# Optimization experiments

Measured on AMD Instinct MI355X. Metric: run time of the kernel, lower is better.

Reference implementation:

```python
import jax, jax.numpy as jnp
import numpy as np

N_ATOMS = 131072
NUM_GS = 128
HIDDEN = 512
N_MOL = 1024


def setup_inputs() -> dict:
    key = jax.random.key(0)
    ks = jax.random.split(key, 16)
    Gs = jax.random.normal(ks[0], (N_ATOMS, NUM_GS), dtype=jnp.float32)
    types = jax.random.randint(ks[1], (N_ATOMS,), 0, 2, dtype=jnp.int32)
    mol_id = jnp.sort(jax.random.randint(ks[2], (N_ATOMS,), 0, N_MOL, dtype=jnp.int32))

    def dense(k, fi, fo):
        return (jax.random.normal(k, (fi, fo), dtype=jnp.float32) / np.float32(np.sqrt(fi)))

    params = {}
    for i, t in enumerate(("A", "B")):
        base = 3 + i * 3
        params[f"W1_{t}"] = dense(ks[base], NUM_GS, HIDDEN)
        params[f"b1_{t}"] = jnp.zeros((HIDDEN,), jnp.float32)
        params[f"W2_{t}"] = dense(ks[base + 1], HIDDEN, HIDDEN)
        params[f"b2_{t}"] = jnp.zeros((HIDDEN,), jnp.float32)
        params[f"W3_{t}"] = dense(ks[base + 2], HIDDEN, 1)
        params[f"b3_{t}"] = jnp.zeros((1,), jnp.float32)
        params[f"off_{t}"] = jnp.zeros((1,), jnp.float32)
    return {"Gs": Gs, "types": types, "mol_id": mol_id, **params}


def _ann(G, W1, b1, W2, b2, W3, b3, off):
    # Atomic NN: two tanh hidden layers, linear scalar output + trainable offset
    h = jnp.tanh(G @ W1 + b1)
    h = jnp.tanh(h @ W2 + b2)
    return (h @ W3 + b3 + off)[:, 0]  # [N]


def reference(Gs, types, mol_id,
              W1_A, b1_A, W2_A, b2_A, W3_A, b3_A, off_A,
              W1_B, b1_B, W2_B, b2_B, W3_B, b3_B, off_B):
    # Per-type expert MLPs; dense-select is the math-equivalent of
    # dynamic_partition -> per-type ANN -> dynamic_stitch for 2 experts.
    eA = _ann(Gs, W1_A, b1_A, W2_A, b2_A, W3_A, b3_A, off_A)
    eB = _ann(Gs, W1_B, b1_B, W2_B, b2_B, W3_B, b3_B, off_B)
    atom_e = jnp.where(types == 0, eA, eB)  # [N_ATOMS]
    # Ragged per-molecule reduce_sum == segment_sum over sorted mol ids
    mol_e = jax.ops.segment_sum(atom_e, mol_id, num_segments=N_MOL)
    counts = jax.ops.segment_sum(jnp.ones_like(atom_e), mol_id, num_segments=N_MOL)
    energy_per_atom = mol_e / jnp.maximum(counts, 1.0)
    return energy_per_atom[:, None]  # [N_MOL, 1]
```

## Files before the change

### kernel.cpp

```cpp
#include <hip/hip_runtime.h>

typedef _Float16 half8  __attribute__((ext_vector_type(8)));
typedef _Float16 half4v __attribute__((ext_vector_type(4)));
typedef __fp16   fp16x2 __attribute__((ext_vector_type(2)));
typedef float    floatx4 __attribute__((ext_vector_type(4)));

#define N_ATOMS 131072
#define NUM_GS  128
#define HIDDEN  512
#define N_MOL   1024

#define BM      64
#define NB_SIDE (N_ATOMS / BM)
#define NT_TOT  (HIDDEN / 16)
#define SH1_LD  (HIDDEN + 8)
#define SGH_LD  (NUM_GS + 8)

#define WS_CNT_OFF     0
#define WS_MOLSUM_OFF  1024
#define WS_PERM_OFF    9216
#define WS_W1FA_OFF    533504
#define WS_W1FB_OFF    664576
#define WS_W2FA_OFF    795648
#define WS_W2FB_OFF    1319936
#define WS_ZERO_BYTES  5120

__device__ __forceinline__ float fast_tanh(float x) {
    float e = exp2f(x * 2.8853900817779268f);
    float r = __builtin_amdgcn_rcpf(e + 1.0f);
    return fmaf(-2.0f, r, 1.0f);
}

__global__ __launch_bounds__(256)
void prep_kernel(const int* __restrict__ types,
                 const float* __restrict__ W1A, const float* __restrict__ W1B,
                 const float* __restrict__ W2A, const float* __restrict__ W2B,
                 int* __restrict__ cnt, int* __restrict__ perm,
                 _Float16* __restrict__ W1FA, _Float16* __restrict__ W1FB,
                 _Float16* __restrict__ W2FA, _Float16* __restrict__ W2FB) {
    __shared__ float tile[32][65];
    const int p   = blockIdx.x;
    const int tid = threadIdx.x;

    if (p < 512) {
        __shared__ int sCA[4];
        __shared__ int sBaseA, sBaseB;
        const int i    = p * 256 + tid;
        const int lane = tid & 63;
        const int w    = tid >> 6;
        const bool isA = (types[i] == 0);
        unsigned long long mask = __ballot(isA);
        unsigned long long lt   = ((unsigned long long)1 << lane) - 1;
        int rA = __popcll(mask & lt);
        if (lane == 0) sCA[w] = __popcll(mask);
        __syncthreads();
        if (tid == 0) {
            int tot = sCA[0] + sCA[1] + sCA[2] + sCA[3];
            sBaseA = atomicAdd(&cnt[0], tot);
            sBaseB = atomicAdd(&cnt[1], 256 - tot);
        }
        __syncthreads();
        int preA = 0;
        #pragma unroll
        for (int k = 0; k < 4; ++k) preA += (k < w) ? sCA[k] : 0;
        int preB = w * 64 - preA;
        int rB   = lane - rA;
        if (isA) perm[sBaseA + preA + rA] = i;
        else     perm[N_ATOMS - 1 - (sBaseB + preB + rB)] = i;
        return;
    }

    const float* src; _Float16* dst; int pb;
    if (p < 544)      { src = W1A; dst = W1FA; pb = p - 512; }
    else if (p < 576) { src = W1B; dst = W1FB; pb = p - 544; }
    else if (p < 704) { src = W2A; dst = W2FA; pb = p - 576; }
    else              { src = W2B; dst = W2FB; pb = p - 704; }
    const int bx = pb & 7;
    const int by = pb >> 3;
    const int n0 = bx * 64, k0 = by * 32;
    #pragma unroll
    for (int i = 0; i < 8; ++i) {
        int idx = tid + i * 256;
        int r = idx >> 6, c = idx & 63;
        tile[r][c] = src[(size_t)(k0 + r) * HIDDEN + n0 + c];
    }
    __syncthreads();
    const int nt_l = tid >> 6, lane = tid & 63;
    const int l15 = lane & 15, q = lane >> 4;
    half8 v;
    #pragma unroll
    for (int j = 0; j < 8; ++j)
        v[j] = (_Float16)tile[q * 8 + j][nt_l * 16 + l15];
    const int ntile = bx * 4 + nt_l;
    *(half8*)(dst + (((size_t)by * NT_TOT + ntile) * 64 + lane) * 8) = v;
}

__global__ __launch_bounds__(512, 4)
void mlp_kernel(const float* __restrict__ Gs,
                const int*   __restrict__ mol_id,
                const _Float16* __restrict__ W1FA, const _Float16* __restrict__ W2FA,
                const float* __restrict__ b1A, const float* __restrict__ b2A,
                const float* __restrict__ W3A, const float* __restrict__ b3A,
                const float* __restrict__ offA,
                const _Float16* __restrict__ W1FB, const _Float16* __restrict__ W2FB,
                const float* __restrict__ b1B, const float* __restrict__ b2B,
                const float* __restrict__ W3B, const float* __restrict__ b3B,
                const float* __restrict__ offB,
                const int* __restrict__ cnt, const int* __restrict__ perm,
                float* __restrict__ mol_sum) {
    __shared__ __align__(16) _Float16 sBuf[BM * SH1_LD];
    __shared__ int   sOrig[BM];
    __shared__ float sPart[8][BM];

    _Float16 (*sH1)[SH1_LD] = (_Float16(*)[SH1_LD])sBuf;
    _Float16 (*sGh)[SGH_LD] = (_Float16(*)[SGH_LD])sBuf;

    const int b     = blockIdx.x;
    const int nA    = cnt[0];
    const int sideB = (b >= NB_SIDE) ? 1 : 0;
    const int r0    = (sideB ? b - NB_SIDE : b) * BM;
    const int nSide = sideB ? (N_ATOMS - nA) : nA;
    if (r0 >= nSide) return;

    const _Float16 *W1F, *W2F;
    const float *b1, *b2, *W3;
    float b3off;
    if (!sideB) { W1F = W1FA; W2F = W2FA; b1 = b1A; b2 = b2A; W3 = W3A; b3off = b3A[0] + offA[0]; }
    else        { W1F = W1FB; W2F = W2FB; b1 = b1B; b2 = b2B; W3 = W3B; b3off = b3B[0] + offB[0]; }

    const int tid  = threadIdx.x;
    const int lane = tid & 63;
    const int wid  = tid >> 6;
    const int l15  = lane & 15;
    const int quad = lane >> 4;

    if (tid < BM) {
        int r = r0 + tid;
        int orig = -1;
        if (r < nSide) orig = sideB ? perm[N_ATOMS - 1 - r] : perm[r];
        sOrig[tid] = orig;
    }

    half8 wa0[4], wa1[4];

    #define LOADW(WF, dst, ks)                                                    \
        {                                                                         \
            _Pragma("unroll")                                                     \
            for (int nt = 0; nt < 4; ++nt)                                        \
                dst[nt] = *(const half8*)((WF) +                                  \
                    (((size_t)(ks) * NT_TOT + wid * 4 + nt) * 64 + lane) * 8);    \
        }

    LOADW(W1F, wa0, 0);

    __syncthreads();

    #pragma unroll
    for (int i = 0; i < 4; ++i) {
        int idx = tid + 512 * i;
        int row = idx >> 5;
        int c4  = idx & 31;
        int orig = sOrig[row];
        float4 v = make_float4(0.f, 0.f, 0.f, 0.f);
        if (orig >= 0) v = ((const float4*)(Gs + (size_t)orig * NUM_GS))[c4];
        union { half4v h4; fp16x2 h2[2]; } hu;
        hu.h2[0] = __builtin_amdgcn_cvt_pkrtz(v.x, v.y);
        hu.h2[1] = __builtin_amdgcn_cvt_pkrtz(v.z, v.w);
        *(half4v*)&sGh[row][c4 * 4] = hu.h4;
    }
    __syncthreads();

    floatx4 acc[4][4];

    #pragma unroll
    for (int nt = 0; nt < 4; ++nt) {
        const float4 bv = *(const float4*)&b1[wid * 64 + nt * 16 + quad * 4];
        #pragma unroll
        for (int mt = 0; mt < 4; ++mt)
            acc[mt][nt] = (floatx4){bv.x, bv.y, bv.z, bv.w};
    }

    #define COMPUTE(SRC, wav, ks)                                                 \
        {                                                                         \
            half8 fb[4];                                                          \
            _Pragma("unroll")                                                     \
            for (int mt = 0; mt < 4; ++mt)                                        \
                fb[mt] = *(const half8*)&SRC[mt * 16 + l15][(ks) * 32 + quad * 8];\
            _Pragma("unroll")                                                     \
            for (int nt = 0; nt < 4; ++nt)                                        \
                _Pragma("unroll")                                                 \
                for (int mt = 0; mt < 4; ++mt)                                    \
                    acc[mt][nt] = __builtin_amdgcn_mfma_f32_16x16x32_f16(         \
                        wav[nt], fb[mt], acc[mt][nt], 0, 0, 0);                   \
        }

    LOADW(W1F, wa1, 1);
    COMPUTE(sGh, wa0, 0);
    LOADW(W1F, wa0, 2);
    COMPUTE(sGh, wa1, 1);
    LOADW(W1F, wa1, 3);
    COMPUTE(sGh, wa0, 2);
    COMPUTE(sGh, wa1, 3);

    LOADW(W2F, wa0, 0);

    __syncthreads();

    #pragma unroll
    for (int mt = 0; mt < 4; ++mt)
        #pragma unroll
        for (int nt = 0; nt < 4; ++nt) {
            float t0 = fast_tanh(acc[mt][nt][0]);
            float t1 = fast_tanh(acc[mt][nt][1]);
            float t2 = fast_tanh(acc[mt][nt][2]);
            float t3 = fast_tanh(acc[mt][nt][3]);
            union { half4v h4; fp16x2 h2[2]; } hu;
            hu.h2[0] = __builtin_amdgcn_cvt_pkrtz(t0, t1);
            hu.h2[1] = __builtin_amdgcn_cvt_pkrtz(t2, t3);
            *(half4v*)&sH1[mt * 16 + l15][wid * 64 + nt * 16 + quad * 4] = hu.h4;
        }
    __syncthreads();

    #pragma unroll
    for (int nt = 0; nt < 4; ++nt) {
        const float4 bv = *(const float4*)&b2[wid * 64 + nt * 16 + quad * 4];
        #pragma unroll
        for (int mt = 0; mt < 4; ++mt)
            acc[mt][nt] = (floatx4){bv.x, bv.y, bv.z, bv.w};
    }

    #pragma unroll 1
    for (int ks = 0; ks < HIDDEN / 32; ks += 2) {
        LOADW(W2F, wa1, ks + 1);
        COMPUTE(sH1, wa0, ks);
        if (ks + 2 < HIDDEN / 32) LOADW(W2F, wa0, ks + 2);
        COMPUTE(sH1, wa1, ks + 1);
    }
    #undef LOADW
    #undef COMPUTE

    float4 w3v[4];
    #pragma unroll
    for (int nt = 0; nt < 4; ++nt)
        w3v[nt] = *(const float4*)&W3[wid * 64 + nt * 16 + quad * 4];

    float p[4] = {0.f, 0.f, 0.f, 0.f};
    #pragma unroll
    for (int mt = 0; mt < 4; ++mt)
        #pragma unroll
        for (int nt = 0; nt < 4; ++nt) {
            p[mt] = fmaf(fast_tanh(acc[mt][nt][0]), w3v[nt].x, p[mt]);
            p[mt] = fmaf(fast_tanh(acc[mt][nt][1]), w3v[nt].y, p[mt]);
            p[mt] = fmaf(fast_tanh(acc[mt][nt][2]), w3v[nt].z, p[mt]);
            p[mt] = fmaf(fast_tanh(acc[mt][nt][3]), w3v[nt].w, p[mt]);
        }
    #pragma unroll
    for (int mt = 0; mt < 4; ++mt) {
        float v = p[mt];
        v += __shfl_xor(v, 16, 64);
        v += __shfl_xor(v, 32, 64);
        if (lane < 16) sPart[wid][mt * 16 + lane] = v;
    }
    __syncthreads();
    if (tid < BM) {
        int orig = sOrig[tid];
        if (orig >= 0) {
            float e = b3off;
            #pragma unroll
            for (int w = 0; w < 8; ++w) e += sPart[w][tid];
            atomicAdd(&mol_sum[mol_id[orig]], e);
        }
    }
}

__global__ void finalize_kernel(const float* __restrict__ mol_sum,
                                const int* __restrict__ mol_id,
                                float* __restrict__ out) {
    int m = blockIdx.x * blockDim.x + threadIdx.x;
    if (m >= N_MOL) return;
    int lo0 = 0, hi0 = N_ATOMS;
    while (lo0 < hi0) { int mid = (lo0 + hi0) >> 1; if (mol_id[mid] < m) lo0 = mid + 1; else hi0 = mid; }
    int lo1 = lo0, hi1 = N_ATOMS;
    while (lo1 < hi1) { int mid = (lo1 + hi1) >> 1; if (mol_id[mid] < m + 1) lo1 = mid + 1; else hi1 = mid; }
    float c = (float)(lo1 - lo0);
    out[m] = mol_sum[m] / fmaxf(c, 1.0f);
}

extern "C" void kernel_launch(void* const* d_in, const int* in_sizes, int n_in,
                              void* d_out, int out_size, void* d_ws, size_t ws_size,
                              hipStream_t stream) {
    const float* Gs     = (const float*)d_in[0];
    const int*   types  = (const int*)d_in[1];
    const int*   mol_id = (const int*)d_in[2];
    const float* W1A = (const float*)d_in[3];
    const float* b1A = (const float*)d_in[4];
    const float* W2A = (const float*)d_in[5];
    const float* b2A = (const float*)d_in[6];
    const float* W3A = (const float*)d_in[7];
    const float* b3A = (const float*)d_in[8];
    const float* oA  = (const float*)d_in[9];
    const float* W1B = (const float*)d_in[10];
    const float* b1B = (const float*)d_in[11];
    const float* W2B = (const float*)d_in[12];
    const float* b2B = (const float*)d_in[13];
    const float* W3B = (const float*)d_in[14];
    const float* b3B = (const float*)d_in[15];
    const float* oB  = (const float*)d_in[16];

    char* ws = (char*)d_ws;
    int*      cnt     = (int*)(ws + WS_CNT_OFF);
    float*    mol_sum = (float*)(ws + WS_MOLSUM_OFF);
    int*      perm    = (int*)(ws + WS_PERM_OFF);
    _Float16* W1FA    = (_Float16*)(ws + WS_W1FA_OFF);
    _Float16* W1FB    = (_Float16*)(ws + WS_W1FB_OFF);
    _Float16* W2FA    = (_Float16*)(ws + WS_W2FA_OFF);
    _Float16* W2FB    = (_Float16*)(ws + WS_W2FB_OFF);
    float* out = (float*)d_out;

    hipMemsetAsync(d_ws, 0, WS_ZERO_BYTES, stream);
    prep_kernel<<<832, 256, 0, stream>>>(types, W1A, W1B, W2A, W2B,
                                         cnt, perm,
                                         W1FA, W1FB, W2FA, W2FB);
    mlp_kernel<<<2 * NB_SIDE, 512, 0, stream>>>(
        Gs, mol_id,
        W1FA, W2FA, b1A, b2A, W3A, b3A, oA,
        W1FB, W2FB, b1B, b2B, W3B, b3B, oB,
        cnt, perm, mol_sum);
    finalize_kernel<<<(N_MOL + 255) / 256, 256, 0, stream>>>(mol_sum, mol_id, out);
}
```

Before: 279.7 us.

## Double row tile to 128 atoms with 1024-thread blocks and narrower per-wave N slices

Raises the per-block atom tile from 64 to 128 rows and uses 16 waves per block. Each wave now covers 32 hidden columns across 8 M-subtiles instead of 64 columns across 4, so every weight fragment loaded from global memory feeds twice as many MFMAs. This halves total weight traffic per atom. The explicit double-buffered weight prefetch is replaced by a simple unroll-2 loop, which risks exposing global load latency. The larger LDS footprint (about 133KB) and 1024-thread blocks may also limit occupancy to one block per CU.

```diff
diff --git a/kernel.cpp b/kernel.cpp
--- a/kernel.cpp
+++ b/kernel.cpp
@@ -10,7 +10,7 @@
 #define HIDDEN  512
 #define N_MOL   1024
 
-#define BM      64
+#define BM      128
 #define NB_SIDE (N_ATOMS / BM)
 #define NT_TOT  (HIDDEN / 16)
 #define SH1_LD  (HIDDEN + 8)
@@ -95,7 +95,7 @@
     *(half8*)(dst + (((size_t)by * NT_TOT + ntile) * 64 + lane) * 8) = v;
 }
 
-__global__ __launch_bounds__(512, 4)
+__global__ __launch_bounds__(1024, 4)
 void mlp_kernel(const float* __restrict__ Gs,
                 const int*   __restrict__ mol_id,
                 const _Float16* __restrict__ W1FA, const _Float16* __restrict__ W2FA,
@@ -110,7 +110,7 @@
                 float* __restrict__ mol_sum) {
     __shared__ __align__(16) _Float16 sBuf[BM * SH1_LD];
     __shared__ int   sOrig[BM];
-    __shared__ float sPart[8][BM];
+    __shared__ float sPart[16][BM];
 
     _Float16 (*sH1)[SH1_LD] = (_Float16(*)[SH1_LD])sBuf;
     _Float16 (*sGh)[SGH_LD] = (_Float16(*)[SGH_LD])sBuf;
@@ -140,24 +140,11 @@
         if (r < nSide) orig = sideB ? perm[N_ATOMS - 1 - r] : perm[r];
         sOrig[tid] = orig;
     }
-
-    half8 wa0[4], wa1[4];
-
-    #define LOADW(WF, dst, ks)                                                    \
-        {                                                                         \
-            _Pragma("unroll")                                                     \
-            for (int nt = 0; nt < 4; ++nt)                                        \
-                dst[nt] = *(const half8*)((WF) +                                  \
-                    (((size_t)(ks) * NT_TOT + wid * 4 + nt) * 64 + lane) * 8);    \
-        }
-
-    LOADW(W1F, wa0, 0);
-
     __syncthreads();
 
     #pragma unroll
     for (int i = 0; i < 4; ++i) {
-        int idx = tid + 512 * i;
+        int idx = tid + 1024 * i;
         int row = idx >> 5;
         int c4  = idx & 31;
         int orig = sOrig[row];
@@ -170,46 +157,54 @@
     }
     __syncthreads();
 
-    floatx4 acc[4][4];
-
-    #pragma unroll
-    for (int nt = 0; nt < 4; ++nt) {
-        const float4 bv = *(const float4*)&b1[wid * 64 + nt * 16 + quad * 4];
-        #pragma unroll
-        for (int mt = 0; mt < 4; ++mt)
+    floatx4 acc[8][2];
+
+    #pragma unroll
+    for (int nt = 0; nt < 2; ++nt) {
+        const float4 bv = *(const float4*)&b1[wid * 32 + nt * 16 + quad * 4];
+        #pragma unroll
+        for (int mt = 0; mt < 8; ++mt)
             acc[mt][nt] = (floatx4){bv.x, bv.y, bv.z, bv.w};
     }
 
+    #define LOADW(WF, dst, ks)                                                    \
+        {                                                                         \
+            _Pragma("unroll")                                                     \
+            for (int nt = 0; nt < 2; ++nt)                                        \
+                dst[nt] = *(const half8*)((WF) +                                  \
+                    (((size_t)(ks) * NT_TOT + wid * 2 + nt) * 64 + lane) * 8);    \
+        }
     #define COMPUTE(SRC, wav, ks)                                                 \
         {                                                                         \
-            half8 fb[4];                                                          \
             _Pragma("unroll")                                                     \
-            for (int mt = 0; mt < 4; ++mt)                                        \
-                fb[mt] = *(const half8*)&SRC[mt * 16 + l15][(ks) * 32 + quad * 8];\
-            _Pragma("unroll")                                                     \
-            for (int nt = 0; nt < 4; ++nt)                                        \
+            for (int hf = 0; hf < 2; ++hf) {                                      \
+                half8 fb[4];                                                      \
                 _Pragma("unroll")                                                 \
-                for (int mt = 0; mt < 4; ++mt)                                    \
-                    acc[mt][nt] = __builtin_amdgcn_mfma_f32_16x16x32_f16(         \
-                        wav[nt], fb[mt], acc[mt][nt], 0, 0, 0);                   \
-        }
-
-    LOADW(W1F, wa1, 1);
-    COMPUTE(sGh, wa0, 0);
-    LOADW(W1F, wa0, 2);
-    COMPUTE(sGh, wa1, 1);
-    LOADW(W1F, wa1, 3);
-    COMPUTE(sGh, wa0, 2);
-    COMPUTE(sGh, wa1, 3);
-
-    LOADW(W2F, wa0, 0);
-
-    __syncthreads();
-
-    #pragma unroll
-    for (int mt = 0; mt < 4; ++mt)
-        #pragma unroll
-        for (int nt = 0; nt < 4; ++nt) {
+                for (int m = 0; m < 4; ++m)                                       \
+                    fb[m] = *(const half8*)&SRC[(hf * 4 + m) * 16 + l15]          \
+                                               [(ks) * 32 + quad * 8];            \
+                _Pragma("unroll")                                                 \
+                for (int nt = 0; nt < 2; ++nt)                                    \
+                    _Pragma("unroll")                                             \
+                    for (int m = 0; m < 4; ++m)                                   \
+                        acc[hf * 4 + m][nt] =                                     \
+                            __builtin_amdgcn_mfma_f32_16x16x32_f16(               \
+                                wav[nt], fb[m], acc[hf * 4 + m][nt], 0, 0, 0);    \
+            }                                                                     \
+        }
+
+    #pragma unroll 2
+    for (int ks = 0; ks < NUM_GS / 32; ++ks) {
+        half8 wa[2];
+        LOADW(W1F, wa, ks);
+        COMPUTE(sGh, wa, ks);
+    }
+    __syncthreads();
+
+    #pragma unroll
+    for (int mt = 0; mt < 8; ++mt)
+        #pragma unroll
+        for (int nt = 0; nt < 2; ++nt) {
             float t0 = fast_tanh(acc[mt][nt][0]);
             float t1 = fast_tanh(acc[mt][nt][1]);
             float t2 = fast_tanh(acc[mt][nt][2]);
@@ -217,45 +212,46 @@
             union { half4v h4; fp16x2 h2[2]; } hu;
             hu.h2[0] = __builtin_amdgcn_cvt_pkrtz(t0, t1);
             hu.h2[1] = __builtin_amdgcn_cvt_pkrtz(t2, t3);
-            *(half4v*)&sH1[mt * 16 + l15][wid * 64 + nt * 16 + quad * 4] = hu.h4;
-        }
-    __syncthreads();
-
-    #pragma unroll
-    for (int nt = 0; nt < 4; ++nt) {
-        const float4 bv = *(const float4*)&b2[wid * 64 + nt * 16 + quad * 4];
-        #pragma unroll
-        for (int mt = 0; mt < 4; ++mt)
+            *(half4v*)&sH1[mt * 16 + l15][wid * 32 + nt * 16 + quad * 4] = hu.h4;
+        }
+    __syncthreads();
+
+    #pragma unroll
+    for (int nt = 0; nt < 2; ++nt) {
+        const float4 bv = *(const float4*)&b2[wid * 32 + nt * 16 + quad * 4];
+        #pragma unroll
+        for (int mt = 0; mt < 8; ++mt)
             acc[mt][nt] = (floatx4){bv.x, bv.y, bv.z, bv.w};
     }
 
-    #pragma unroll 1
-    for (int ks = 0; ks < HIDDEN / 32; ks += 2) {
-        LOADW(W2F, wa1, ks + 1);
-        COMPUTE(sH1, wa0, ks);
-        if (ks + 2 < HIDDEN / 32) LOADW(W2F, wa0, ks + 2);
-        COMPUTE(sH1, wa1, ks + 1);
+    #pragma unroll 2
+    for (int ks = 0; ks < HIDDEN / 32; ++ks) {
+        half8 wa[2];
+        LOADW(W2F, wa, ks);
+        COMPUTE(sH1, wa, ks);
     }
     #undef LOADW
     #undef COMPUTE
 
-    float4 w3v[4];
-    #pragma unroll
-    for (int nt = 0; nt < 4; ++nt)
-        w3v[nt] = *(const float4*)&W3[wid * 64 + nt * 16 + quad * 4];
-
-    float p[4] = {0.f, 0.f, 0.f, 0.f};
-    #pragma unroll
-    for (int mt = 0; mt < 4; ++mt)
-        #pragma unroll
-        for (int nt = 0; nt < 4; ++nt) {
+    float4 w3v[2];
+    #pragma unroll
+    for (int nt = 0; nt < 2; ++nt)
+        w3v[nt] = *(const float4*)&W3[wid * 32 + nt * 16 + quad * 4];
+
+    float p[8];
+    #pragma unroll
+    for (int mt = 0; mt < 8; ++mt) p[mt] = 0.f;
+    #pragma unroll
+    for (int mt = 0; mt < 8; ++mt)
+        #pragma unroll
+        for (int nt = 0; nt < 2; ++nt) {
             p[mt] = fmaf(fast_tanh(acc[mt][nt][0]), w3v[nt].x, p[mt]);
             p[mt] = fmaf(fast_tanh(acc[mt][nt][1]), w3v[nt].y, p[mt]);
             p[mt] = fmaf(fast_tanh(acc[mt][nt][2]), w3v[nt].z, p[mt]);
             p[mt] = fmaf(fast_tanh(acc[mt][nt][3]), w3v[nt].w, p[mt]);
         }
     #pragma unroll
-    for (int mt = 0; mt < 4; ++mt) {
+    for (int mt = 0; mt < 8; ++mt) {
         float v = p[mt];
         v += __shfl_xor(v, 16, 64);
         v += __shfl_xor(v, 32, 64);
@@ -267,7 +263,7 @@
         if (orig >= 0) {
             float e = b3off;
             #pragma unroll
-            for (int w = 0; w < 8; ++w) e += sPart[w][tid];
+            for (int w = 0; w < 16; ++w) e += sPart[w][tid];
             atomicAdd(&mol_sum[mol_id[orig]], e);
         }
     }
@@ -321,7 +317,7 @@
     prep_kernel<<<832, 256, 0, stream>>>(types, W1A, W1B, W2A, W2B,
                                          cnt, perm,
                                          W1FA, W1FB, W2FA, W2FB);
-    mlp_kernel<<<2 * NB_SIDE, 512, 0, stream>>>(
+    mlp_kernel<<<2 * NB_SIDE, 1024, 0, stream>>>(
         Gs, mol_id,
         W1FA, W2FA, b1A, b2A, W3A, b3A, oA,
         W1FB, W2FB, b1B, b2B, W3B, b3B, oB,
```

Result: slower. 310.8 us (+11.1%).

## Replace atomic partition with deterministic scan and simplify weight prefetch loop

Applied to the files above, without the earlier changes.

The type partition now runs in three kernels: per-block A counts, a single-block exclusive scan over them, and a scatter pass. This replaces the atomicAdd-based permutation, so perm becomes deterministic and blocks stay in atom order, which may improve Gs locality in the MLP. The MLP loops also drop the manual double-buffered weight register prefetch in favour of per-step loads with compiler unrolling, and split the MFMA inner block into halves, which should lower register pressure. The cost is two extra kernel launches and weaker explicit overlap of weight loads with MFMAs.

```diff
diff --git a/kernel.cpp b/kernel.cpp
--- a/kernel.cpp
+++ b/kernel.cpp
@@ -18,12 +18,13 @@
 
 #define WS_CNT_OFF     0
 #define WS_MOLSUM_OFF  1024
+#define WS_CNTBUF_OFF  5120
+#define WS_BASEA_OFF   7168
 #define WS_PERM_OFF    9216
 #define WS_W1FA_OFF    533504
 #define WS_W1FB_OFF    664576
 #define WS_W2FA_OFF    795648
 #define WS_W2FB_OFF    1319936
-#define WS_ZERO_BYTES  5120
 
 __device__ __forceinline__ float fast_tanh(float x) {
     float e = exp2f(x * 2.8853900817779268f);
@@ -32,41 +33,26 @@
 }
 
 __global__ __launch_bounds__(256)
-void prep_kernel(const int* __restrict__ types,
-                 const float* __restrict__ W1A, const float* __restrict__ W1B,
-                 const float* __restrict__ W2A, const float* __restrict__ W2B,
-                 int* __restrict__ cnt, int* __restrict__ perm,
-                 _Float16* __restrict__ W1FA, _Float16* __restrict__ W1FB,
-                 _Float16* __restrict__ W2FA, _Float16* __restrict__ W2FB) {
+void prepA_kernel(const int* __restrict__ types,
+                  const float* __restrict__ W1A, const float* __restrict__ W1B,
+                  const float* __restrict__ W2A, const float* __restrict__ W2B,
+                  int* __restrict__ cntbuf,
+                  _Float16* __restrict__ W1FA, _Float16* __restrict__ W1FB,
+                  _Float16* __restrict__ W2FA, _Float16* __restrict__ W2FB) {
     __shared__ float tile[32][65];
     const int p   = blockIdx.x;
     const int tid = threadIdx.x;
 
     if (p < 512) {
         __shared__ int sCA[4];
-        __shared__ int sBaseA, sBaseB;
         const int i    = p * 256 + tid;
         const int lane = tid & 63;
         const int w    = tid >> 6;
         const bool isA = (types[i] == 0);
         unsigned long long mask = __ballot(isA);
-        unsigned long long lt   = ((unsigned long long)1 << lane) - 1;
-        int rA = __popcll(mask & lt);
         if (lane == 0) sCA[w] = __popcll(mask);
         __syncthreads();
-        if (tid == 0) {
-            int tot = sCA[0] + sCA[1] + sCA[2] + sCA[3];
-            sBaseA = atomicAdd(&cnt[0], tot);
-            sBaseB = atomicAdd(&cnt[1], 256 - tot);
-        }
-        __syncthreads();
-        int preA = 0;
-        #pragma unroll
-        for (int k = 0; k < 4; ++k) preA += (k < w) ? sCA[k] : 0;
-        int preB = w * 64 - preA;
-        int rB   = lane - rA;
-        if (isA) perm[sBaseA + preA + rA] = i;
-        else     perm[N_ATOMS - 1 - (sBaseB + preB + rB)] = i;
+        if (tid == 0) cntbuf[p] = sCA[0] + sCA[1] + sCA[2] + sCA[3];
         return;
     }
 
@@ -93,6 +79,53 @@
         v[j] = (_Float16)tile[q * 8 + j][nt_l * 16 + l15];
     const int ntile = bx * 4 + nt_l;
     *(half8*)(dst + (((size_t)by * NT_TOT + ntile) * 64 + lane) * 8) = v;
+}
+
+__global__ __launch_bounds__(512)
+void prepB_kernel(const int* __restrict__ cntbuf,
+                  int* __restrict__ baseA, int* __restrict__ cnt) {
+    __shared__ int s[512];
+    const int tid = threadIdx.x;
+    const int c = cntbuf[tid];
+    s[tid] = c;
+    __syncthreads();
+    #pragma unroll
+    for (int off = 1; off < 512; off <<= 1) {
+        int v = s[tid];
+        int add = (tid >= off) ? s[tid - off] : 0;
+        __syncthreads();
+        s[tid] = v + add;
+        __syncthreads();
+    }
+    baseA[tid] = s[tid] - c;
+    if (tid == 511) { cnt[0] = s[511]; cnt[1] = N_ATOMS - s[511]; }
+}
+
+__global__ __launch_bounds__(256)
+void prepC_kernel(const int* __restrict__ types,
+                  const int* __restrict__ baseA,
+                  int* __restrict__ perm) {
+    __shared__ int sCA[4];
+    const int p    = blockIdx.x;
+    const int tid  = threadIdx.x;
+    const int i    = p * 256 + tid;
+    const int lane = tid & 63;
+    const int w    = tid >> 6;
+    const bool isA = (types[i] == 0);
+    unsigned long long mask = __ballot(isA);
+    unsigned long long lt   = ((unsigned long long)1 << lane) - 1;
+    int rA = __popcll(mask & lt);
+    if (lane == 0) sCA[w] = __popcll(mask);
+    __syncthreads();
+    int preA = 0;
+    #pragma unroll
+    for (int k = 0; k < 4; ++k) preA += (k < w) ? sCA[k] : 0;
+    const int bA = baseA[p];
+    const int bB = p * 256 - bA;
+    int preB = w * 64 - preA;
+    int rB   = lane - rA;
+    if (isA) perm[bA + preA + rA] = i;
+    else     perm[N_ATOMS - 1 - (bB + preB + rB)] = i;
 }
 
 __global__ __launch_bounds__(512, 4)
@@ -140,19 +173,6 @@
         if (r < nSide) orig = sideB ? perm[N_ATOMS - 1 - r] : perm[r];
         sOrig[tid] = orig;
     }
-
-    half8 wa0[4], wa1[4];
-
-    #define LOADW(WF, dst, ks)                                                    \
-        {                                                                         \
-            _Pragma("unroll")                                                     \
-            for (int nt = 0; nt < 4; ++nt)                                        \
-                dst[nt] = *(const half8*)((WF) +                                  \
-                    (((size_t)(ks) * NT_TOT + wid * 4 + nt) * 64 + lane) * 8);    \
-        }
-
-    LOADW(W1F, wa0, 0);
-
     __syncthreads();
 
     #pragma unroll
@@ -180,30 +200,38 @@
             acc[mt][nt] = (floatx4){bv.x, bv.y, bv.z, bv.w};
     }
 
+    #define LOADW(WF, dst, ks)                                                    \
+        {                                                                         \
+            _Pragma("unroll")                                                     \
+            for (int nt = 0; nt < 4; ++nt)                                        \
+                dst[nt] = *(const half8*)((WF) +                                  \
+                    (((size_t)(ks) * NT_TOT + wid * 4 + nt) * 64 + lane) * 8);    \
+        }
     #define COMPUTE(SRC, wav, ks)                                                 \
         {                                                                         \
-            half8 fb[4];                                                          \
             _Pragma("unroll")                                                     \
-            for (int mt = 0; mt < 4; ++mt)                                        \
-                fb[mt] = *(const half8*)&SRC[mt * 16 + l15][(ks) * 32 + quad * 8];\
-            _Pragma("unroll")                                                     \
-            for (int nt = 0; nt < 4; ++nt)                                        \
+            for (int hf = 0; hf < 2; ++hf) {                                      \
+                half8 fb[2];                                                      \
                 _Pragma("unroll")                                                 \
-                for (int mt = 0; mt < 4; ++mt)                                    \
-                    acc[mt][nt] = __builtin_amdgcn_mfma_f32_16x16x32_f16(         \
-                        wav[nt], fb[mt], acc[mt][nt], 0, 0, 0);                   \
-        }
-
-    LOADW(W1F, wa1, 1);
-    COMPUTE(sGh, wa0, 0);
-    LOADW(W1F, wa0, 2);
-    COMPUTE(sGh, wa1, 1);
-    LOADW(W1F, wa1, 3);
-    COMPUTE(sGh, wa0, 2);
-    COMPUTE(sGh, wa1, 3);
-
-    LOADW(W2F, wa0, 0);
-
+                for (int m = 0; m < 2; ++m)                                       \
+                    fb[m] = *(const half8*)&SRC[(hf * 2 + m) * 16 + l15]          \
+                                               [(ks) * 32 + quad * 8];            \
+                _Pragma("unroll")                                                 \
+                for (int nt = 0; nt < 4; ++nt)                                    \
+                    _Pragma("unroll")                                             \
+                    for (int m = 0; m < 2; ++m)                                   \
+                        acc[hf * 2 + m][nt] =                                     \
+                            __builtin_amdgcn_mfma_f32_16x16x32_f16(               \
+                                wav[nt], fb[m], acc[hf * 2 + m][nt], 0, 0, 0);    \
+            }                                                                     \
+        }
+
+    #pragma unroll
+    for (int ks = 0; ks < NUM_GS / 32; ++ks) {
+        half8 wa[4];
+        LOADW(W1F, wa, ks);
+        COMPUTE(sGh, wa, ks);
+    }
     __syncthreads();
 
     #pragma unroll
@@ -229,12 +257,11 @@
             acc[mt][nt] = (floatx4){bv.x, bv.y, bv.z, bv.w};
     }
 
-    #pragma unroll 1
-    for (int ks = 0; ks < HIDDEN / 32; ks += 2) {
-        LOADW(W2F, wa1, ks + 1);
-        COMPUTE(sH1, wa0, ks);
-        if (ks + 2 < HIDDEN / 32) LOADW(W2F, wa0, ks + 2);
-        COMPUTE(sH1, wa1, ks + 1);
+    #pragma unroll 2
+    for (int ks = 0; ks < HIDDEN / 32; ++ks) {
+        half8 wa[4];
+        LOADW(W2F, wa, ks);
+        COMPUTE(sH1, wa, ks);
     }
     #undef LOADW
     #undef COMPUTE
@@ -310,6 +337,8 @@
     char* ws = (char*)d_ws;
     int*      cnt     = (int*)(ws + WS_CNT_OFF);
     float*    mol_sum = (float*)(ws + WS_MOLSUM_OFF);
+    int*      cntbuf  = (int*)(ws + WS_CNTBUF_OFF);
+    int*      baseA   = (int*)(ws + WS_BASEA_OFF);
     int*      perm    = (int*)(ws + WS_PERM_OFF);
     _Float16* W1FA    = (_Float16*)(ws + WS_W1FA_OFF);
     _Float16* W1FB    = (_Float16*)(ws + WS_W1FB_OFF);
@@ -317,10 +346,12 @@
     _Float16* W2FB    = (_Float16*)(ws + WS_W2FB_OFF);
     float* out = (float*)d_out;
 
-    hipMemsetAsync(d_ws, 0, WS_ZERO_BYTES, stream);
-    prep_kernel<<<832, 256, 0, stream>>>(types, W1A, W1B, W2A, W2B,
-                                         cnt, perm,
-                                         W1FA, W1FB, W2FA, W2FB);
+    hipMemsetAsync(mol_sum, 0, N_MOL * sizeof(float), stream);
+    prepA_kernel<<<832, 256, 0, stream>>>(types, W1A, W1B, W2A, W2B,
+                                          cntbuf,
+                                          W1FA, W1FB, W2FA, W2FB);
+    prepB_kernel<<<1, 512, 0, stream>>>(cntbuf, baseA, cnt);
+    prepC_kernel<<<512, 256, 0, stream>>>(types, baseA, perm);
     mlp_kernel<<<2 * NB_SIDE, 512, 0, stream>>>(
         Gs, mol_id,
         W1FA, W2FA, b1A, b2A, W3A, b3A, oA,
```

New measurement: 291.5 us. 1.04x slower.
